# Kernel optimization log

Measured on AMD Instinct MI355X. Metric: run time of the kernel, lower is better.

The kernel has to match this reference:

```python
import jax, jax.numpy as jnp
import numpy as np

GRID_SIZE = 16
SPLINE_ORDER = 4
GRID_LO, GRID_HI = -1.0, 1.0
NUM_GRID = 2 * SPLINE_ORDER + GRID_SIZE + 1  # 25 knots
NUM_COEFFS = GRID_SIZE + SPLINE_ORDER        # 20 basis functions
B, IN_F, OUT_F = 2048, 512, 512


def _make_grid():
    h = (GRID_HI - GRID_LO) / GRID_SIZE
    t1 = -SPLINE_ORDER * h + GRID_LO
    t2 = (GRID_SIZE + SPLINE_ORDER + 1) * h + GRID_LO
    return jnp.linspace(t1, t2, NUM_GRID)


def _bspline_basis(x, grid):
    # x: [..., in]; returns [..., in, NUM_COEFFS] via De Boor recursion
    xe = x[..., None]
    bases = ((xe >= grid[:-1]) & (xe < grid[1:])).astype(x.dtype)
    for k in range(1, SPLINE_ORDER + 1):
        left = (xe - grid[:-k - 1]) / (grid[k:-1] - grid[:-k - 1]) * bases[..., :-1]
        right = (grid[k + 1:] - xe) / (grid[k + 1:] - grid[1:-k]) * bases[..., 1:]
        bases = left + right
    return bases


def setup_inputs() -> dict:
    key = jax.random.key(0)
    ks = jax.random.split(key, 5)
    fan = np.sqrt(1.0 / IN_F)
    return {
        "x": jax.random.normal(ks[0], (B, IN_F), jnp.float32),
        "prelu_weight": jax.random.normal(ks[1], (OUT_F, IN_F), jnp.float32) * 0.25,
        "base_weight": jax.random.uniform(ks[2], (OUT_F, IN_F), jnp.float32, -fan, fan),
        "spline_weight": jax.random.uniform(ks[3], (OUT_F, IN_F), jnp.float32, -fan, fan),
        "spline_coeffs": jax.random.normal(ks[4], (OUT_F, IN_F, NUM_COEFFS), jnp.float32) * 0.1,
    }


def reference(x, prelu_weight, base_weight, spline_weight, spline_coeffs):
    grid = _make_grid()
    xc = jnp.clip(x, GRID_LO, GRID_HI)
    pos = jax.nn.relu(xc)
    neg = xc - pos
    # base path: sum_j base_w[i,j]*(prelu_w[i,j]*neg[b,j] + pos[b,j])
    # fused: never materialize the [out, B, in] prelu output
    base = neg @ (base_weight * prelu_weight).T + pos @ base_weight.T  # [B, out]
    basis = _bspline_basis(xc, grid)  # [B, in, K]
    # spline path: fold spline_weight into coeffs, single contraction over (j,k)
    eff_coeffs = spline_weight[:, :, None] * spline_coeffs  # [out, in, K]
    spline = jnp.einsum('bjk,ijk->bi', basis, eff_coeffs)   # [B, out]
    return base + spline
```

## Files before the change

kernel.cpp:

```cpp
#include <hip/hip_runtime.h>


typedef _Float16 half_t;
typedef __attribute__((ext_vector_type(8))) _Float16 half8;
typedef __attribute__((ext_vector_type(4))) float floatx4;

#define B_DIM   2048
#define J_DIM   512
#define O_DIM   512
#define SLOT32  32
#define KT32    (J_DIM * SLOT32)
#define BM      256
#define BN      256
#define KSPLIT  16
#define NPH     16

__device__ __forceinline__ void bspline5(float xc, int& k0, float Nv[5]) {
    const float invS = 7.68f;
    float u = (xc + 1.5f) * invS;
    int m = (int)u;
    m = min(max(m, 3), 19);
    k0 = m - 4;
    Nv[0] = 1.f; Nv[1] = 0.f; Nv[2] = 0.f; Nv[3] = 0.f; Nv[4] = 0.f;
#pragma unroll
    for (int d = 1; d <= 4; ++d) {
        float nw[5];
        float inv_d = 1.0f / (float)d;
#pragma unroll
        for (int r = 0; r < 5; ++r) {
            if (r > d) { nw[r] = 0.f; continue; }
            float kk = (float)(m - d + r);
            float acc = 0.f;
            if (r >= 1) acc += (u - kk) * Nv[r - 1];
            if (r < d)  acc += (kk + (float)(d + 1) - u) * Nv[r];
            nw[r] = acc * inv_d;
        }
#pragma unroll
        for (int r = 0; r < 5; ++r) Nv[r] = nw[r];
    }
}

__device__ __forceinline__ unsigned packh2(float a, float b) {
    half_t ha = (half_t)a, hb = (half_t)b;
    unsigned short ua = __builtin_bit_cast(unsigned short, ha);
    unsigned short ub = __builtin_bit_cast(unsigned short, hb);
    return (unsigned)ua | ((unsigned)ub << 16);
}

__global__ __launch_bounds__(256) void prep_c32(const float* __restrict__ pw,
                                                const float* __restrict__ bw,
                                                const float* __restrict__ sw,
                                                const float* __restrict__ sc,
                                                half_t* __restrict__ Ct) {
    int bid = blockIdx.x;
    int t = threadIdx.x;
    int sub = t >> 7;
    int jq  = t & 127;
    int j0  = jq * 4;

    int i = bid * 2 + sub;
    size_t ij0 = (size_t)i * J_DIM + j0;
    float4 s4 = *(const float4*)(sw + ij0);
    float4 b4 = *(const float4*)(bw + ij0);
    float4 p4 = *(const float4*)(pw + ij0);
    const float4* sp4 = (const float4*)(sc + ij0 * 20);
    unsigned u[64];
#pragma unroll
    for (int jj = 0; jj < 4; ++jj) {
        float s = ((const float*)&s4)[jj];
        float b = ((const float*)&b4)[jj];
        float p = ((const float*)&p4)[jj];
#pragma unroll
        for (int v = 0; v < 5; ++v) {
            float4 c4 = sp4[jj * 5 + v];
            u[jj * 16 + v * 2 + 0] = packh2(s * c4.x, s * c4.y);
            u[jj * 16 + v * 2 + 1] = packh2(s * c4.z, s * c4.w);
        }
        u[jj * 16 + 10] = packh2(b * p, b);
#pragma unroll
        for (int v = 11; v < 16; ++v) u[jj * 16 + v] = 0u;
    }
    uint4* dst = (uint4*)(Ct + (size_t)i * KT32 + (size_t)j0 * SLOT32);
#pragma unroll
    for (int v = 0; v < 16; ++v)
        dst[v] = make_uint4(u[4 * v], u[4 * v + 1], u[4 * v + 2], u[4 * v + 3]);
}

__global__ __launch_bounds__(512, 2) void kan_fused(const float* __restrict__ x,
                                                    const half_t* __restrict__ Ct,
                                                    float* __restrict__ out) {
    __shared__ float  xt[32 * 256];
    __shared__ half_t As[2][BM * 64];
    __shared__ half_t Bs[2][BN * 64];

    int lid = blockIdx.x + 8 * (blockIdx.y + 2 * blockIdx.z);
    int c8 = lid & 7;
    int r2 = lid >> 3;
    int bz = c8 + 8 * (r2 & 1);
    int rr2 = r2 >> 1;
    int bx = rr2 & 7;
    int by = rr2 >> 3;

    int m0 = bx * BM;
    int n0 = by * BN;
    int j0 = bz * 32;

    int t = threadIdx.x;
    int w = t >> 6, l = t & 63;
    int wm = w >> 2, wn = w & 3;
    int q = l >> 4, fr = l & 15;

    const half_t* gB = Ct + (size_t)n0 * KT32 + (size_t)j0 * SLOT32;

    int srow8 = l >> 3;
    int lq    = (l & 7) ^ (srow8 & 7);

    floatx4 acc[8][4] = {};

#define ISSUE_BS(p, buf)                                                      \
    {                                                                         \
        _Pragma("unroll")                                                     \
        for (int s = 0; s < 4; ++s) {                                         \
            int rB = w * 32 + s * 8 + srow8;                                  \
            __builtin_amdgcn_global_load_lds(                                 \
                (const __attribute__((address_space(1))) unsigned int*)       \
                    (gB + (size_t)rB * KT32 + (p) * 64 + lq * 8),             \
                (__attribute__((address_space(3))) unsigned int*)             \
                    (&Bs[buf][(w * 32 + s * 8) * 64]),                        \
                16, 0, 0);                                                    \
        }                                                                     \
    }

#define GEN_AS(p, buf)                                                        \
    {                                                                         \
        int bl = t & 255, jp = t >> 8;                                        \
        int rx = bl & 7;                                                      \
        float xv = xt[((p) * 2 + jp) * 256 + bl];                             \
        float xc = fminf(fmaxf(xv, -1.f), 1.f);                               \
        float pos = fmaxf(xc, 0.f);                                           \
        float neg = xc - pos;                                                 \
        int k0; float Nv[5];                                                  \
        bspline5(xc, k0, Nv);                                                 \
        half_t* rb = &As[buf][bl * 64];                                       \
        half8 z8 = {};                                                        \
        _Pragma("unroll")                                                     \
        for (int kq = 0; kq < 4; ++kq)                                        \
            *(half8*)(rb + ((jp * 4 + kq) ^ rx) * 8) = z8;                    \
        *(unsigned*)(rb + ((jp * 4 + 2) ^ rx) * 8 + 4) = packh2(neg, pos);    \
        _Pragma("unroll")                                                     \
        for (int rr = 0; rr < 5; ++rr) {                                      \
            int k = k0 + rr;                                                  \
            if (k >= 0)                                                       \
                rb[(((jp * 4 + (k >> 3)) ^ rx) * 8) + (k & 7)] =              \
                    (half_t)Nv[rr];                                           \
        }                                                                     \
    }

    ISSUE_BS(0, 0)
#pragma unroll
    for (int v = 0; v < 4; ++v) {
        int r = v * 64 + (t >> 3);
        int cq = t & 7;
        float4 xv4 = *(const float4*)(x + (size_t)(m0 + r) * J_DIM + j0 + cq * 4);
#pragma unroll
        for (int c = 0; c < 4; ++c)
            xt[(cq * 4 + c) * 256 + r] = ((const float*)&xv4)[c];
    }
    __syncthreads();
    GEN_AS(0, 0)

    for (int p = 0; p < NPH; ++p) {
        asm volatile("s_waitcnt vmcnt(0) lgkmcnt(0)" ::: "memory");
        __builtin_amdgcn_s_barrier();

        if (p + 1 < NPH) ISSUE_BS(p + 1, (p + 1) & 1)

        const half_t* Ab = &As[p & 1][0];
        const half_t* Bb = &Bs[p & 1][0];
#pragma unroll
        for (int ks = 0; ks < 2; ++ks) {
            half8 af[8], bf[4];
#pragma unroll
            for (int nt = 0; nt < 4; ++nt)
                bf[nt] = *(const half8*)(Bb + (wn * 64 + nt * 16 + fr) * 64
                                            + (((ks * 4 + q) ^ (fr & 7)) * 8));
#pragma unroll
            for (int mt = 0; mt < 8; ++mt)
                af[mt] = *(const half8*)(Ab + (wm * 128 + mt * 16 + fr) * 64
                                            + (((ks * 4 + q) ^ (fr & 7)) * 8));
            __builtin_amdgcn_s_setprio(1);
#pragma unroll
            for (int mt = 0; mt < 8; ++mt)
#pragma unroll
                for (int nt = 0; nt < 4; ++nt)
                    acc[mt][nt] = __builtin_amdgcn_mfma_f32_16x16x32_f16(
                        af[mt], bf[nt], acc[mt][nt], 0, 0, 0);
            __builtin_amdgcn_s_setprio(0);
        }
        if (p + 1 < NPH) GEN_AS(p + 1, (p + 1) & 1)
    }
#undef GEN_AS
#undef ISSUE_BS

    float* dst = out + (size_t)bz * ((size_t)B_DIM * O_DIM);
#pragma unroll
    for (int mt = 0; mt < 8; ++mt)
#pragma unroll
        for (int nt = 0; nt < 4; ++nt) {
            int rw = m0 + wm * 128 + mt * 16 + q * 4;
            int cc = n0 + wn * 64 + nt * 16 + fr;
#pragma unroll
            for (int rg = 0; rg < 4; ++rg)
                dst[(size_t)(rw + rg) * O_DIM + cc] = acc[mt][nt][rg];
        }
}

__global__ __launch_bounds__(256) void reduce16(const float* __restrict__ parts,
                                                float* __restrict__ out) {
    constexpr int N4 = B_DIM * O_DIM / 4;
    int i = blockIdx.x * 256 + threadIdx.x;
    const float4* p = (const float4*)parts;
    float4 a = p[i];
#pragma unroll
    for (int z = 1; z < KSPLIT; ++z) {
        float4 b = p[(size_t)z * N4 + i];
        a.x += b.x; a.y += b.y; a.z += b.z; a.w += b.w;
    }
    ((float4*)out)[i] = a;
}

__global__ __launch_bounds__(256) void kan_fallback(const float* __restrict__ x,
                                                    const float* __restrict__ pw,
                                                    const float* __restrict__ bw,
                                                    const float* __restrict__ sw,
                                                    const float* __restrict__ sc,
                                                    float* __restrict__ out) {
    __shared__ float s_neg[J_DIM], s_pos[J_DIM], s_bas[J_DIM][5];
    __shared__ int s_k0[J_DIM];
    int b = blockIdx.x;
    int t = threadIdx.x;
#pragma unroll
    for (int jj = 0; jj < 2; ++jj) {
        int j = t + jj * 256;
        float xv = x[(size_t)b * J_DIM + j];
        float xc = fminf(fmaxf(xv, -1.f), 1.f);
        float pos = fmaxf(xc, 0.f);
        s_pos[j] = pos;
        s_neg[j] = xc - pos;
        int k0; float Nv[5];
        bspline5(xc, k0, Nv);
        s_k0[j] = k0;
#pragma unroll
        for (int r = 0; r < 5; ++r) s_bas[j][r] = Nv[r];
    }
    __syncthreads();
    for (int i = t; i < O_DIM; i += 256) {
        float acc = 0.f;
        for (int j = 0; j < J_DIM; ++j) {
            size_t ij = (size_t)i * J_DIM + j;
            float bwv = bw[ij];
            acc += bwv * (pw[ij] * s_neg[j] + s_pos[j]);
            int k0 = s_k0[j];
            const float* cp = sc + ij * 20;
            float sp = 0.f;
#pragma unroll
            for (int r = 0; r < 5; ++r) {
                int k = k0 + r;
                if (k >= 0) sp += s_bas[j][r] * cp[k];
            }
            acc += sw[ij] * sp;
        }
        out[(size_t)b * O_DIM + i] = acc;
    }
}

extern "C" void kernel_launch(void* const* d_in, const int* in_sizes, int n_in,
                              void* d_out, int out_size, void* d_ws, size_t ws_size,
                              hipStream_t stream) {
    const float* x  = (const float*)d_in[0];
    const float* pw = (const float*)d_in[1];
    const float* bw = (const float*)d_in[2];
    const float* sw = (const float*)d_in[3];
    const float* sc = (const float*)d_in[4];
    float* out = (float*)d_out;

    const size_t ct32_bytes  = (size_t)O_DIM * KT32 * sizeof(half_t);
    const size_t parts_bytes = (size_t)KSPLIT * B_DIM * O_DIM * sizeof(float);

    if (ws_size >= ct32_bytes + parts_bytes) {
        half_t* Ct32 = (half_t*)d_ws;
        float* parts = (float*)((char*)d_ws + ct32_bytes);

        prep_c32<<<O_DIM / 2, 256, 0, stream>>>(pw, bw, sw, sc, Ct32);
        dim3 g(B_DIM / BM, O_DIM / BN, KSPLIT);
        kan_fused<<<g, 512, 0, stream>>>(x, Ct32, parts);
        reduce16<<<(B_DIM * O_DIM / 4) / 256, 256, 0, stream>>>(parts, out);
    } else {
        kan_fallback<<<B_DIM, 256, 0, stream>>>(x, pw, bw, sw, sc, out);
    }
}
```

Measured before the change: 148.2 us.

## Triple-buffer B tiles with partial vmcnt waits and per-thread x prefetch

The main GEMM loop is fully unrolled with three B-tile LDS buffers, so weight tiles are issued two phases ahead and each barrier waits only for the oldest loads (partial vmcnt) instead of draining all memory traffic. The x transposition through shared memory is removed; each thread instead loads its own x values from global memory into registers several phases early. prep_c32 is also remapped to one thread per (i,j) with more blocks, which gives more parallelism but narrower loads. The extra B buffer raises LDS use, which may threaten two blocks per CU, and the vmcnt counts must match the interleaved x loads exactly.

```diff
diff --git a/kernel.cpp b/kernel.cpp
--- a/kernel.cpp
+++ b/kernel.cpp
@@ -13,7 +13,6 @@
 #define BM      256
 #define BN      256
 #define KSPLIT  16
-#define NPH     16
 
 __device__ __forceinline__ void bspline5(float xc, int& k0, float Nv[5]) {
     const float invS = 7.68f;
@@ -53,45 +52,32 @@
                                                 const float* __restrict__ sc,
                                                 half_t* __restrict__ Ct) {
     int bid = blockIdx.x;
-    int t = threadIdx.x;
-    int sub = t >> 7;
-    int jq  = t & 127;
-    int j0  = jq * 4;
-
-    int i = bid * 2 + sub;
-    size_t ij0 = (size_t)i * J_DIM + j0;
-    float4 s4 = *(const float4*)(sw + ij0);
-    float4 b4 = *(const float4*)(bw + ij0);
-    float4 p4 = *(const float4*)(pw + ij0);
-    const float4* sp4 = (const float4*)(sc + ij0 * 20);
-    unsigned u[64];
-#pragma unroll
-    for (int jj = 0; jj < 4; ++jj) {
-        float s = ((const float*)&s4)[jj];
-        float b = ((const float*)&b4)[jj];
-        float p = ((const float*)&p4)[jj];
-#pragma unroll
-        for (int v = 0; v < 5; ++v) {
-            float4 c4 = sp4[jj * 5 + v];
-            u[jj * 16 + v * 2 + 0] = packh2(s * c4.x, s * c4.y);
-            u[jj * 16 + v * 2 + 1] = packh2(s * c4.z, s * c4.w);
-        }
-        u[jj * 16 + 10] = packh2(b * p, b);
-#pragma unroll
-        for (int v = 11; v < 16; ++v) u[jj * 16 + v] = 0u;
-    }
-    uint4* dst = (uint4*)(Ct + (size_t)i * KT32 + (size_t)j0 * SLOT32);
-#pragma unroll
-    for (int v = 0; v < 16; ++v)
+    int i = bid >> 1;
+    int j = ((bid & 1) << 8) + threadIdx.x;
+    size_t ij = (size_t)i * J_DIM + j;
+    float s = sw[ij], b = bw[ij], p = pw[ij];
+    const float4* sp4 = (const float4*)(sc + ij * 20);
+    unsigned u[16];
+#pragma unroll
+    for (int v = 0; v < 5; ++v) {
+        float4 c4 = sp4[v];
+        u[v * 2 + 0] = packh2(s * c4.x, s * c4.y);
+        u[v * 2 + 1] = packh2(s * c4.z, s * c4.w);
+    }
+    u[10] = packh2(b * p, b);
+#pragma unroll
+    for (int v = 11; v < 16; ++v) u[v] = 0u;
+    uint4* dst = (uint4*)(Ct + (size_t)i * KT32 + (size_t)j * SLOT32);
+#pragma unroll
+    for (int v = 0; v < 4; ++v)
         dst[v] = make_uint4(u[4 * v], u[4 * v + 1], u[4 * v + 2], u[4 * v + 3]);
 }
 
 __global__ __launch_bounds__(512, 2) void kan_fused(const float* __restrict__ x,
                                                     const half_t* __restrict__ Ct,
                                                     float* __restrict__ out) {
-    __shared__ float  xt[32 * 256];
     __shared__ half_t As[2][BM * 64];
-    __shared__ half_t Bs[2][BN * 64];
+    __shared__ half_t Bs[3][BN * 64];
 
     int lid = blockIdx.x + 8 * (blockIdx.y + 2 * blockIdx.z);
     int c8 = lid & 7;
@@ -111,9 +97,11 @@
     int q = l >> 4, fr = l & 15;
 
     const half_t* gB = Ct + (size_t)n0 * KT32 + (size_t)j0 * SLOT32;
-
     int srow8 = l >> 3;
-    int lq    = (l & 7) ^ (srow8 & 7);
+    int lq    = (l & 7) ^ srow8;
+
+    int bl = t & 255, jp = t >> 8;
+    const float* xb = x + (size_t)(m0 + bl) * J_DIM + j0 + jp;
 
     floatx4 acc[8][4] = {};
 
@@ -131,16 +119,14 @@
         }                                                                     \
     }
 
-#define GEN_AS(p, buf)                                                        \
+#define GEN_AS(buf, XV)                                                       \
     {                                                                         \
-        int bl = t & 255, jp = t >> 8;                                        \
         int rx = bl & 7;                                                      \
-        float xv = xt[((p) * 2 + jp) * 256 + bl];                             \
-        float xc = fminf(fmaxf(xv, -1.f), 1.f);                               \
-        float pos = fmaxf(xc, 0.f);                                           \
-        float neg = xc - pos;                                                 \
+        float xcl = fminf(fmaxf((XV), -1.f), 1.f);                            \
+        float pos = fmaxf(xcl, 0.f);                                          \
+        float neg = xcl - pos;                                                \
         int k0; float Nv[5];                                                  \
-        bspline5(xc, k0, Nv);                                                 \
+        bspline5(xcl, k0, Nv);                                                \
         half_t* rb = &As[buf][bl * 64];                                       \
         half8 z8 = {};                                                        \
         _Pragma("unroll")                                                     \
@@ -156,49 +142,65 @@
         }                                                                     \
     }
 
+#define MMPH(apar, bsi)                                                       \
+    {                                                                         \
+        const half_t* Ab = &As[apar][0];                                      \
+        const half_t* Bb = &Bs[bsi][0];                                       \
+        _Pragma("unroll")                                                     \
+        for (int ks = 0; ks < 2; ++ks) {                                      \
+            half8 af[8], bf[4];                                               \
+            _Pragma("unroll")                                                 \
+            for (int nt = 0; nt < 4; ++nt)                                    \
+                bf[nt] = *(const half8*)(Bb + (wn * 64 + nt * 16 + fr) * 64   \
+                                            + (((ks * 4 + q) ^ (fr & 7)) * 8));\
+            _Pragma("unroll")                                                 \
+            for (int mt = 0; mt < 8; ++mt)                                    \
+                af[mt] = *(const half8*)(Ab + (wm * 128 + mt * 16 + fr) * 64  \
+                                            + (((ks * 4 + q) ^ (fr & 7)) * 8));\
+            __builtin_amdgcn_s_setprio(1);                                    \
+            _Pragma("unroll")                                                 \
+            for (int mt = 0; mt < 8; ++mt)                                    \
+                _Pragma("unroll")                                             \
+                for (int nt = 0; nt < 4; ++nt)                                \
+                    acc[mt][nt] = __builtin_amdgcn_mfma_f32_16x16x32_f16(     \
+                        af[mt], bf[nt], acc[mt][nt], 0, 0, 0);                \
+            __builtin_amdgcn_s_setprio(0);                                    \
+        }                                                                     \
+    }
+
+#define PWAIT(VN)                                                             \
+    asm volatile("s_waitcnt vmcnt(" #VN ")" ::: "memory");                    \
+    __builtin_amdgcn_s_barrier();
+#define LGKM0 asm volatile("s_waitcnt lgkmcnt(0)" ::: "memory");
+
+    float xv0 = xb[0],  xv1 = xb[2],  xv2 = xb[4];
+    float xv3 = xb[6],  xv4 = xb[8],  xv5 = xb[10];
+    float xv6, xv7, xv8, xv9, xv10, xv11, xv12, xv13, xv14, xv15;
     ISSUE_BS(0, 0)
-#pragma unroll
-    for (int v = 0; v < 4; ++v) {
-        int r = v * 64 + (t >> 3);
-        int cq = t & 7;
-        float4 xv4 = *(const float4*)(x + (size_t)(m0 + r) * J_DIM + j0 + cq * 4);
-#pragma unroll
-        for (int c = 0; c < 4; ++c)
-            xt[(cq * 4 + c) * 256 + r] = ((const float*)&xv4)[c];
-    }
-    __syncthreads();
-    GEN_AS(0, 0)
-
-    for (int p = 0; p < NPH; ++p) {
-        asm volatile("s_waitcnt vmcnt(0) lgkmcnt(0)" ::: "memory");
-        __builtin_amdgcn_s_barrier();
-
-        if (p + 1 < NPH) ISSUE_BS(p + 1, (p + 1) & 1)
-
-        const half_t* Ab = &As[p & 1][0];
-        const half_t* Bb = &Bs[p & 1][0];
-#pragma unroll
-        for (int ks = 0; ks < 2; ++ks) {
-            half8 af[8], bf[4];
-#pragma unroll
-            for (int nt = 0; nt < 4; ++nt)
-                bf[nt] = *(const half8*)(Bb + (wn * 64 + nt * 16 + fr) * 64
-                                            + (((ks * 4 + q) ^ (fr & 7)) * 8));
-#pragma unroll
-            for (int mt = 0; mt < 8; ++mt)
-                af[mt] = *(const half8*)(Ab + (wm * 128 + mt * 16 + fr) * 64
-                                            + (((ks * 4 + q) ^ (fr & 7)) * 8));
-            __builtin_amdgcn_s_setprio(1);
-#pragma unroll
-            for (int mt = 0; mt < 8; ++mt)
-#pragma unroll
-                for (int nt = 0; nt < 4; ++nt)
-                    acc[mt][nt] = __builtin_amdgcn_mfma_f32_16x16x32_f16(
-                        af[mt], bf[nt], acc[mt][nt], 0, 0, 0);
-            __builtin_amdgcn_s_setprio(0);
-        }
-        if (p + 1 < NPH) GEN_AS(p + 1, (p + 1) & 1)
-    }
+    ISSUE_BS(1, 1)
+    GEN_AS(0, xv0)
+    LGKM0
+
+    PWAIT(4)  ISSUE_BS(2, 2)   xv6  = xb[12]; MMPH(0, 0) GEN_AS(1, xv1)  LGKM0
+    PWAIT(5)  ISSUE_BS(3, 0)   xv7  = xb[14]; MMPH(1, 1) GEN_AS(0, xv2)  LGKM0
+    PWAIT(6)  ISSUE_BS(4, 1)   xv8  = xb[16]; MMPH(0, 2) GEN_AS(1, xv3)  LGKM0
+    PWAIT(6)  ISSUE_BS(5, 2)   xv9  = xb[18]; MMPH(1, 0) GEN_AS(0, xv4)  LGKM0
+    PWAIT(6)  ISSUE_BS(6, 0)   xv10 = xb[20]; MMPH(0, 1) GEN_AS(1, xv5)  LGKM0
+    PWAIT(6)  ISSUE_BS(7, 1)   xv11 = xb[22]; MMPH(1, 2) GEN_AS(0, xv6)  LGKM0
+    PWAIT(6)  ISSUE_BS(8, 2)   xv12 = xb[24]; MMPH(0, 0) GEN_AS(1, xv7)  LGKM0
+    PWAIT(6)  ISSUE_BS(9, 0)   xv13 = xb[26]; MMPH(1, 1) GEN_AS(0, xv8)  LGKM0
+    PWAIT(6)  ISSUE_BS(10, 1)  xv14 = xb[28]; MMPH(0, 2) GEN_AS(1, xv9)  LGKM0
+    PWAIT(6)  ISSUE_BS(11, 2)  xv15 = xb[30]; MMPH(1, 0) GEN_AS(0, xv10) LGKM0
+    PWAIT(6)  ISSUE_BS(12, 0)                 MMPH(0, 1) GEN_AS(1, xv11) LGKM0
+    PWAIT(5)  ISSUE_BS(13, 1)                 MMPH(1, 2) GEN_AS(0, xv12) LGKM0
+    PWAIT(4)  ISSUE_BS(14, 2)                 MMPH(0, 0) GEN_AS(1, xv13) LGKM0
+    PWAIT(4)  ISSUE_BS(15, 0)                 MMPH(1, 1) GEN_AS(0, xv14) LGKM0
+    PWAIT(4)                                  MMPH(0, 2) GEN_AS(1, xv15) LGKM0
+    PWAIT(0)                                  MMPH(1, 0)
+
+#undef PWAIT
+#undef LGKM0
+#undef MMPH
 #undef GEN_AS
 #undef ISSUE_BS
 
@@ -291,7 +293,7 @@
         half_t* Ct32 = (half_t*)d_ws;
         float* parts = (float*)((char*)d_ws + ct32_bytes);
 
-        prep_c32<<<O_DIM / 2, 256, 0, stream>>>(pw, bw, sw, sc, Ct32);
+        prep_c32<<<O_DIM * 2, 256, 0, stream>>>(pw, bw, sw, sc, Ct32);
         dim3 g(B_DIM / BM, O_DIM / BN, KSPLIT);
         kan_fused<<<g, 512, 0, stream>>>(x, Ct32, parts);
         reduce16<<<(B_DIM * O_DIM / 4) / 256, 256, 0, stream>>>(parts, out);
```

New measurement: 138.4 us. 1.07x faster.
